# Kernel optimization log

Hardware: AMD Instinct MI355X
Metric: run time of the kernel (lower is better)

Reference implementation:

```python
import jax, jax.numpy as jnp
import numpy as np

# nodes per graph before / after pool1 / after pool2 (111, ceil(.5*111)=56, ceil(.5*56)=28)
N0, N1, N2 = 111, 56, 28


def _gcn(x, adj, w):
    n = x.shape[1]
    a = adj + jnp.eye(n, dtype=x.dtype)
    d = a.sum(-1)
    dis = jnp.where(d > 0, jax.lax.rsqrt(d), 0.0)
    an = dis[:, :, None] * a * dis[:, None, :]
    return jnp.einsum('bij,bjf->bif', an, x @ w)


def _cheb(x, adj, wk):
    # ChebConv K=3 (the 'sp' spectral branch; K=3 is set in __init__), lmax=2
    # => scaled Laplacian L_hat = L - I = -D^-1/2 A D^-1/2
    d = adj.sum(-1)
    dis = jnp.where(d > 0, jax.lax.rsqrt(d), 0.0)
    lh = -(dis[:, :, None] * adj * dis[:, None, :])
    t1 = jnp.einsum('bij,bjf->bif', lh, x)
    t2 = 2.0 * jnp.einsum('bij,bjf->bif', lh, t1) - x
    return x @ wk[0] + t1 @ wk[1] + t2 @ wk[2]


def _pool(x, adj, k):
    # HGPSLPool (sl=False): node information score = ||(I - D^-1 A) x||_1 per node,
    # top-k node selection per graph, induced subgraph on the kept nodes.
    d = adj.sum(-1)
    dinv = jnp.where(d > 0, 1.0 / d, 0.0)
    h = x - dinv[..., None] * jnp.einsum('bij,bjf->bif', adj, x)
    score = jnp.abs(h).sum(-1)                      # [B, N]
    _, idx = jax.lax.top_k(score, k)                # [B, k]
    xp = jnp.take_along_axis(x, idx[..., None], axis=1)
    rows = jnp.take_along_axis(adj, idx[..., None], axis=1)
    adjp = jnp.take_along_axis(rows, idx[:, None, :], axis=2)
    return xp, adjp


def _readout(h):
    # cat[global_max_pool, global_mean_pool] over the node axis
    return jnp.concatenate([h.max(axis=1), h.mean(axis=1)], axis=-1)


def _forward(x, adj, w_gcn1, w_sp1, w_gcn2, w_sp2, lin1_w, lin1_b, lin2_w, lin2_b):
    xm = jax.nn.relu(_gcn(x, adj, w_gcn1))
    xp = jax.nn.relu(_cheb(x, adj, w_sp1))
    h = jnp.concatenate([xm, xp], axis=-1)          # [B, 111, 256]
    h, adj1 = _pool(h, adj, N1)                     # [B, 56, 256]
    x1 = _readout(h)                                # [B, 512]
    xm = jax.nn.relu(_gcn(h, adj1, w_gcn2))
    xp = jax.nn.relu(_cheb(h, adj1, w_sp2))
    h = jnp.concatenate([xm, xp], axis=-1)          # [B, 56, 256]
    h, adj2 = _pool(h, adj1, N2)                    # [B, 28, 256]
    x2 = _readout(h)                                # [B, 512]
    flat = h.reshape(h.shape[0], -1)                # [B, 28*256]
    z = jnp.concatenate([flat, x1, x2], axis=-1)    # [B, 8192]
    f = jax.nn.relu(z @ lin1_w + lin1_b)
    features = jax.nn.relu(f @ lin2_w + lin2_b)
    x_lo = jax.nn.softmax(features, axis=-1)
    return x_lo, features


def setup_inputs() -> dict:
    B, F, D2, NHID = 2048, 111, 128, 256
    key = jax.random.key(0)
    ks = jax.random.split(key, 8)
    x = jax.random.normal(ks[0], (B, N0, F), jnp.float32)
    u = jax.random.uniform(ks[1], (B, N0, N0), jnp.float32)
    a = (u < 0.15).astype(jnp.float32)
    adj = jnp.maximum(a, jnp.transpose(a, (0, 2, 1))) * (1.0 - jnp.eye(N0, dtype=jnp.float32))
    s = 0.05
    w_gcn1 = jax.random.normal(ks[2], (F, D2), jnp.float32) * s
    w_sp1 = jax.random.normal(ks[3], (3, F, D2), jnp.float32) * s
    w_gcn2 = jax.random.normal(ks[4], (2 * D2, D2), jnp.float32) * s
    w_sp2 = jax.random.normal(ks[5], (3, 2 * D2, D2), jnp.float32) * s
    din = (N2 + 4) * 2 * D2  # 8192: flattened pooled nodes + two max/mean readouts
    lin1_w = jax.random.normal(ks[6], (din, NHID), jnp.float32) * s
    lin1_b = jnp.zeros((NHID,), jnp.float32)
    lin2_w = jax.random.normal(ks[7], (NHID, NHID // 2), jnp.float32) * s
    lin2_b = jnp.zeros((NHID // 2,), jnp.float32)
    return {'x': x, 'adj': adj, 'w_gcn1': w_gcn1, 'w_sp1': w_sp1, 'w_gcn2': w_gcn2,
            'w_sp2': w_sp2, 'lin1_w': lin1_w, 'lin1_b': lin1_b, 'lin2_w': lin2_w, 'lin2_b': lin2_b}


def reference(x, adj, w_gcn1, w_sp1, w_gcn2, w_sp2, lin1_w, lin1_b, lin2_w, lin2_b):
    return _forward(x, adj, w_gcn1, w_sp1, w_gcn2, w_sp2, lin1_w, lin1_b, lin2_w, lin2_b)
```

## Files before the change

kernel.cpp:

```cpp
#include <hip/hip_runtime.h>
#include <hip/hip_bf16.h>

#define NB   2048
#define NN0  111
#define NN1  56
#define NN2  28
#define FD   256
#define HD   128

__global__ __launch_bounds__(512, 2) void k_stage1(
    const float* __restrict__ x, const float* __restrict__ adj,
    const float* __restrict__ wg, const float* __restrict__ wsp,
    float* __restrict__ h1, int* __restrict__ selb,
    unsigned long long* __restrict__ adjp, int b0)
{
  extern __shared__ float sm[];
  float* xs   = sm;
  float* bufw = xs + 12432;
  unsigned* abits = (unsigned*)(bufw + 14336);
  float* dis0 = (float*)(abits + 448);
  float* dis1 = dis0 + 112;
  float* dinv = dis1 + 112;
  float* sc   = dinv + 112;
  int*   sel  = (int*)(sc + 112);

  const int tid  = threadIdx.x;
  const int lane = tid & 63;
  const int wv   = tid >> 6;
  const int bl   = blockIdx.x;
  const int b    = b0 + bl;
  const float* xb = x   + (size_t)b * (NN0 * NN0);
  const float* ab = adj + (size_t)b * (NN0 * NN0);

  for (int idx = tid; idx < NN0 * NN0; idx += 512) {
    int i = idx / NN0, k = idx - i * NN0;
    xs[i * 112 + k] = xb[idx];
  }
  if (tid < 128) bufw[111 * 128 + tid] = 0.0f;
  for (int i = wv; i < NN0; i += 8) {
    unsigned long long m0 = __ballot(ab[i * NN0 + lane] != 0.0f);
    float a1v = (64 + lane < NN0) ? ab[i * NN0 + 64 + lane] : 0.0f;
    unsigned long long m1 = __ballot(a1v != 0.0f);
    if (lane == 0) {
      abits[i * 4 + 0] = (unsigned)m0; abits[i * 4 + 1] = (unsigned)(m0 >> 32);
      abits[i * 4 + 2] = (unsigned)m1; abits[i * 4 + 3] = (unsigned)(m1 >> 32);
      int d = __popcll(m0) + __popcll(m1);
      dis0[i] = (d > 0) ? (1.0f / sqrtf((float)d)) : 0.0f;
      dis1[i] = 1.0f / sqrtf((float)(d + 1));
      dinv[i] = (d > 0) ? (1.0f / (float)d) : 0.0f;
    }
  }
  __syncthreads();

  auto nsum2 = [&](int i) {
    const unsigned* rb = abits + i * 4;
    unsigned lo0 = (unsigned)__builtin_amdgcn_readfirstlane(rb[0]);
    unsigned hi0 = (unsigned)__builtin_amdgcn_readfirstlane(rb[1]);
    unsigned lo1 = (unsigned)__builtin_amdgcn_readfirstlane(rb[2]);
    unsigned hi1 = (unsigned)__builtin_amdgcn_readfirstlane(rb[3]);
    unsigned long long u0 = ((unsigned long long)hi0 << 32) | (unsigned long long)lo0;
    unsigned long long u1 = ((unsigned long long)hi1 << 32) | (unsigned long long)lo1;
    float2 s0 = {0,0}, s1 = {0,0}, s2 = {0,0}, s3 = {0,0};
    while (u0 | u1) {
      int j0 = u0 ? (int)__builtin_ctzll(u0) : 111; u0 &= u0 - 1;
      int j1 = u0 ? (int)__builtin_ctzll(u0) : 111; u0 &= u0 - 1;
      int j2 = u1 ? (int)(64 + __builtin_ctzll(u1)) : 111; u1 &= u1 - 1;
      int j3 = u1 ? (int)(64 + __builtin_ctzll(u1)) : 111; u1 &= u1 - 1;
      float2 p0 = *(const float2*)&bufw[j0 * 128 + 2 * lane];
      float2 p1 = *(const float2*)&bufw[j1 * 128 + 2 * lane];
      float2 p2 = *(const float2*)&bufw[j2 * 128 + 2 * lane];
      float2 p3 = *(const float2*)&bufw[j3 * 128 + 2 * lane];
      s0.x += p0.x; s0.y += p0.y; s1.x += p1.x; s1.y += p1.y;
      s2.x += p2.x; s2.y += p2.y; s3.x += p3.x; s3.y += p3.y;
    }
    return make_float2((s0.x + s1.x) + (s2.x + s3.x),
                       (s0.y + s1.y) + (s2.y + s3.y));
  };

  float* h1b = h1 + (size_t)bl * (NN0 * FD);

  {
    float aG0[14], aG1[14];
    float a2r[2][14], a1r[2][14], a0r[2][14];
#pragma unroll
    for (int t = 0; t < 14; ++t) {
      aG0[t] = 0.f; aG1[t] = 0.f;
      a2r[0][t] = 0.f; a2r[1][t] = 0.f;
      a1r[0][t] = 0.f; a1r[1][t] = 0.f;
      a0r[0][t] = 0.f; a0r[1][t] = 0.f;
    }
    const float* pG = wg  + 2 * lane;
    const float* p2 = wsp + 2 * (NN0 * HD) + 2 * lane;
    const float* p1 = wsp + 1 * (NN0 * HD) + 2 * lane;
    const float* p0 = wsp + 2 * lane;
    for (int kq = 0; kq < 27; ++kq) {
      int k0 = kq * 4;
      float2 g[4], s2[4], u1w[4], v0[4];
#pragma unroll
      for (int j = 0; j < 4; ++j) {
        g[j]   = *(const float2*)&pG[(k0 + j) * HD];
        s2[j]  = *(const float2*)&p2[(k0 + j) * HD];
        u1w[j] = *(const float2*)&p1[(k0 + j) * HD];
        v0[j]  = *(const float2*)&p0[(k0 + j) * HD];
      }
#pragma unroll
      for (int t = 0; t < 14; ++t) {
        int r = wv + 8 * t;
        if (r < NN0) {
          float4 xq = *(const float4*)(xs + r * 112 + k0);
          aG0[t]    += xq.x*g[0].x   + xq.y*g[1].x   + xq.z*g[2].x   + xq.w*g[3].x;
          aG1[t]    += xq.x*g[0].y   + xq.y*g[1].y   + xq.z*g[2].y   + xq.w*g[3].y;
          a2r[0][t] += xq.x*s2[0].x  + xq.y*s2[1].x  + xq.z*s2[2].x  + xq.w*s2[3].x;
          a2r[1][t] += xq.x*s2[0].y  + xq.y*s2[1].y  + xq.z*s2[2].y  + xq.w*s2[3].y;
          a1r[0][t] += xq.x*u1w[0].x + xq.y*u1w[1].x + xq.z*u1w[2].x + xq.w*u1w[3].x;
          a1r[1][t] += xq.x*u1w[0].y + xq.y*u1w[1].y + xq.z*u1w[2].y + xq.w*u1w[3].y;
          a0r[0][t] += xq.x*v0[0].x  + xq.y*v0[1].x  + xq.z*v0[2].x  + xq.w*v0[3].x;
          a0r[1][t] += xq.x*v0[0].y  + xq.y*v0[1].y  + xq.z*v0[2].y  + xq.w*v0[3].y;
        }
      }
    }
#pragma unroll
    for (int k = 108; k < 111; ++k) {
      float2 gv = *(const float2*)&pG[k * HD];
      float2 sv = *(const float2*)&p2[k * HD];
      float2 uv = *(const float2*)&p1[k * HD];
      float2 vv = *(const float2*)&p0[k * HD];
#pragma unroll
      for (int t = 0; t < 14; ++t) {
        int r = wv + 8 * t;
        if (r < NN0) {
          float xv = xs[r * 112 + k];
          aG0[t]    += xv * gv.x; aG1[t]    += xv * gv.y;
          a2r[0][t] += xv * sv.x; a2r[1][t] += xv * sv.y;
          a1r[0][t] += xv * uv.x; a1r[1][t] += xv * uv.y;
          a0r[0][t] += xv * vv.x; a0r[1][t] += xv * vv.y;
        }
      }
    }
#pragma unroll
    for (int t = 0; t < 14; ++t) {
      int r = wv + 8 * t;
      if (r < NN0) {
        float d1 = dis1[r];
        *(float2*)&bufw[r * 128 + 2 * lane] = make_float2(d1 * aG0[t], d1 * aG1[t]);
      }
    }
    __syncthreads();

    for (int t = 0; t < 14; ++t) {
      int i = wv + 8 * t;
      if (i < NN0) {
        float2 self = *(const float2*)&bufw[i * 128 + 2 * lane];
        float2 ns = nsum2(i);
        float d1 = dis1[i];
        float2 o = make_float2(fmaxf(d1 * (self.x + ns.x), 0.f),
                               fmaxf(d1 * (self.y + ns.y), 0.f));
        *(float2*)&h1b[i * FD + 2 * lane] = o;
      }
    }
    __syncthreads();
#pragma unroll
    for (int t = 0; t < 14; ++t) {
      int r = wv + 8 * t;
      if (r < NN0) {
        float d0r = dis0[r];
        *(float2*)&bufw[r * 128 + 2 * lane] = make_float2(d0r * a2r[0][t], d0r * a2r[1][t]);
      }
    }
    __syncthreads();
    float2 ur[14], cacc[14];
    for (int t = 0; t < 14; ++t) {
      int i = wv + 8 * t;
      if (i < NN0) {
        float2 ns = nsum2(i);
        float sc0 = -dis0[i] * dis0[i];
        ur[t] = make_float2(sc0 * ns.x, sc0 * ns.y);
        cacc[t] = make_float2(-a2r[0][t], -a2r[1][t]);
      } else { ur[t] = make_float2(0.f, 0.f); cacc[t] = make_float2(0.f, 0.f); }
    }
    __syncthreads();
#pragma unroll
    for (int t = 0; t < 14; ++t) {
      int r = wv + 8 * t;
      if (r < NN0) *(float2*)&bufw[r * 128 + 2 * lane] = ur[t];
    }
    __syncthreads();
    for (int t = 0; t < 14; ++t) {
      int i = wv + 8 * t;
      if (i < NN0) {
        float2 ns = nsum2(i);
        float d0i = dis0[i];
        cacc[t].x -= 2.0f * d0i * ns.x;
        cacc[t].y -= 2.0f * d0i * ns.y;
      }
    }
    __syncthreads();
#pragma unroll
    for (int t = 0; t < 14; ++t) {
      int r = wv + 8 * t;
      if (r < NN0) {
        float d0r = dis0[r];
        *(float2*)&bufw[r * 128 + 2 * lane] = make_float2(d0r * a1r[0][t], d0r * a1r[1][t]);
      }
    }
    __syncthreads();
    for (int t = 0; t < 14; ++t) {
      int i = wv + 8 * t;
      if (i < NN0) {
        float2 ns = nsum2(i);
        float d0i = dis0[i];
        float2 o = make_float2(fmaxf(cacc[t].x - d0i * ns.x + a0r[0][t], 0.f),
                               fmaxf(cacc[t].y - d0i * ns.y + a0r[1][t], 0.f));
        *(float2*)&h1b[i * FD + HD + 2 * lane] = o;
      }
    }
  }
  __syncthreads();

  float sA[14];
#pragma unroll
  for (int t = 0; t < 14; ++t) {
    int r = wv + 8 * t;
    if (r < NN0)
      *(float2*)&bufw[r * 128 + 2 * lane] = *(const float2*)&h1b[r * FD + 2 * lane];
  }
  __syncthreads();
  for (int t = 0; t < 14; ++t) {
    int i = wv + 8 * t;
    if (i < NN0) {
      float2 self = *(const float2*)&bufw[i * 128 + 2 * lane];
      float2 nb = nsum2(i);
      float di = dinv[i];
      sA[t] = fabsf(self.x - di * nb.x) + fabsf(self.y - di * nb.y);
    } else sA[t] = 0.f;
  }
  __syncthreads();
#pragma unroll
  for (int t = 0; t < 14; ++t) {
    int r = wv + 8 * t;
    if (r < NN0)
      *(float2*)&bufw[r * 128 + 2 * lane] = *(const float2*)&h1b[r * FD + HD + 2 * lane];
  }
  __syncthreads();
  for (int t = 0; t < 14; ++t) {
    int i = wv + 8 * t;
    if (i < NN0) {
      float2 self = *(const float2*)&bufw[i * 128 + 2 * lane];
      float2 nb = nsum2(i);
      float di = dinv[i];
      float s = sA[t] + fabsf(self.x - di * nb.x) + fabsf(self.y - di * nb.y);
      for (int off = 32; off; off >>= 1) s += __shfl_xor(s, off);
      if (lane == 0) sc[i] = s;
    }
  }
  __syncthreads();
  if (tid < NN0) {
    float my = sc[tid];
    int cnt = 0;
    for (int j = 0; j < NN0; ++j) {
      float sj = sc[j];
      cnt += (sj > my) || (sj == my && j < tid);
    }
    if (cnt < NN1) sel[cnt] = tid;
  }
  __syncthreads();
  for (int r = wv; r < NN1; r += 8) {
    int i = sel[r];
    int j2 = (lane < NN1) ? sel[lane] : 0;
    bool bit = (lane < NN1) && ((abits[i * 4 + (j2 >> 5)] >> (j2 & 31)) & 1);
    unsigned long long m = __ballot(bit);
    if (lane == 0) adjp[(size_t)bl * NN1 + r] = m;
  }
  if (tid < NN1) selb[(size_t)bl * NN1 + tid] = sel[tid];
}

__global__ __launch_bounds__(512, 2) void k_stage2(
    const float* __restrict__ h1, const int* __restrict__ selb,
    const unsigned long long* __restrict__ adjp,
    const float* __restrict__ wg, const float* __restrict__ wsp,
    float* __restrict__ zbuf)
{
  extern __shared__ float sm[];
  float* hs   = sm;
  float* bufw = hs + 14592;
  unsigned long long* rowm = (unsigned long long*)(bufw + 7296);
  float* dis0 = (float*)(rowm + 56);
  float* dis1 = dis0 + 64;
  float* dinv = dis1 + 64;
  float* sc   = dinv + 64;
  int* sel2   = (int*)(sc + 64);
  int* seli   = sel2 + 32;

  const int tid = threadIdx.x, lane = tid & 63, wv = tid >> 6;
  const int bl = blockIdx.x;
  const float* h1b = h1 + (size_t)bl * (NN0 * FD);
  float* zb = zbuf + (size_t)bl * 8192;

  if (tid < NN1) seli[tid] = selb[(size_t)bl * NN1 + tid];
  if (tid < 128) bufw[56 * 128 + tid] = 0.0f;
  if (tid < 256) hs[56 * 256 + tid] = 0.0f;
  if (tid < NN1) {
    unsigned long long m = adjp[(size_t)bl * NN1 + tid];
    rowm[tid] = m;
    int d = __popcll(m);
    dis0[tid] = (d > 0) ? (1.0f / sqrtf((float)d)) : 0.0f;
    dis1[tid] = 1.0f / sqrtf((float)(d + 1));
    dinv[tid] = (d > 0) ? (1.0f / (float)d) : 0.0f;
  }
  __syncthreads();
  for (int q = tid; q < NN1 * 64; q += 512) {
    int row = q >> 6, c = q & 63;
    ((float4*)hs)[row * 64 + c] =
        ((const float4*)(h1b + (size_t)seli[row] * FD))[c];
  }
  __syncthreads();
  if (tid < FD) {
    float mx = -3.402823466e38f, sm2 = 0.0f;
    for (int r = 0; r < NN1; ++r) {
      float v = hs[r * 256 + tid];
      mx = fmaxf(mx, v); sm2 += v;
    }
    zb[7168 + tid] = mx;
    zb[7424 + tid] = sm2 / 56.0f;
  }

  auto nsum2 = [&](int i) {
    unsigned long long m = rowm[i];
    unsigned lo = (unsigned)__builtin_amdgcn_readfirstlane((unsigned)m);
    unsigned hi = (unsigned)__builtin_amdgcn_readfirstlane((unsigned)(m >> 32));
    unsigned long long u = ((unsigned long long)hi << 32) | (unsigned long long)lo;
    float2 s0 = {0,0}, s1 = {0,0}, s2 = {0,0}, s3 = {0,0};
    while (u) {
      int j0 = (int)__builtin_ctzll(u); u &= u - 1;
      int j1 = u ? (int)__builtin_ctzll(u) : 56; u &= u - 1;
      int j2 = u ? (int)__builtin_ctzll(u) : 56; u &= u - 1;
      int j3 = u ? (int)__builtin_ctzll(u) : 56; u &= u - 1;
      float2 p0 = *(const float2*)&bufw[j0 * 128 + 2 * lane];
      float2 p1 = *(const float2*)&bufw[j1 * 128 + 2 * lane];
      float2 p2 = *(const float2*)&bufw[j2 * 128 + 2 * lane];
      float2 p3 = *(const float2*)&bufw[j3 * 128 + 2 * lane];
      s0.x += p0.x; s0.y += p0.y; s1.x += p1.x; s1.y += p1.y;
      s2.x += p2.x; s2.y += p2.y; s3.x += p3.x; s3.y += p3.y;
    }
    return make_float2((s0.x + s1.x) + (s2.x + s3.x),
                       (s0.y + s1.y) + (s2.y + s3.y));
  };
  auto nsum_hs = [&](int i, int base) {
    unsigned long long m = rowm[i];
    unsigned lo = (unsigned)__builtin_amdgcn_readfirstlane((unsigned)m);
    unsigned hi = (unsigned)__builtin_amdgcn_readfirstlane((unsigned)(m >> 32));
    unsigned long long u = ((unsigned long long)hi << 32) | (unsigned long long)lo;
    float2 s0 = {0,0}, s1 = {0,0}, s2 = {0,0}, s3 = {0,0};
    while (u) {
      int j0 = (int)__builtin_ctzll(u); u &= u - 1;
      int j1 = u ? (int)__builtin_ctzll(u) : 56; u &= u - 1;
      int j2 = u ? (int)__builtin_ctzll(u) : 56; u &= u - 1;
      int j3 = u ? (int)__builtin_ctzll(u) : 56; u &= u - 1;
      float2 p0 = *(const float2*)&hs[j0 * 256 + base + 2 * lane];
      float2 p1 = *(const float2*)&hs[j1 * 256 + base + 2 * lane];
      float2 p2 = *(const float2*)&hs[j2 * 256 + base + 2 * lane];
      float2 p3 = *(const float2*)&hs[j3 * 256 + base + 2 * lane];
      s0.x += p0.x; s0.y += p0.y; s1.x += p1.x; s1.y += p1.y;
      s2.x += p2.x; s2.y += p2.y; s3.x += p3.x; s3.y += p3.y;
    }
    return make_float2((s0.x + s1.x) + (s2.x + s3.x),
                       (s0.y + s1.y) + (s2.y + s3.y));
  };

  float aG0[7], aG1[7];
  float a2r[2][7], a1r[2][7], a0r[2][7];
#pragma unroll
  for (int t = 0; t < 7; ++t) {
    aG0[t] = 0.f; aG1[t] = 0.f;
    a2r[0][t] = 0.f; a2r[1][t] = 0.f;
    a1r[0][t] = 0.f; a1r[1][t] = 0.f;
    a0r[0][t] = 0.f; a0r[1][t] = 0.f;
  }
  {
    const float* pG = wg  + 2 * lane;
    const float* p2 = wsp + 2 * (FD * HD) + 2 * lane;
    const float* p1 = wsp + 1 * (FD * HD) + 2 * lane;
    const float* p0 = wsp + 2 * lane;
    for (int kq = 0; kq < 64; ++kq) {
      int k0 = kq * 4;
      float2 g[4], s2[4], u1w[4], v0[4];
#pragma unroll
      for (int j = 0; j < 4; ++j) {
        g[j]   = *(const float2*)&pG[(k0 + j) * HD];
        s2[j]  = *(const float2*)&p2[(k0 + j) * HD];
        u1w[j] = *(const float2*)&p1[(k0 + j) * HD];
        v0[j]  = *(const float2*)&p0[(k0 + j) * HD];
      }
#pragma unroll
      for (int t = 0; t < 7; ++t) {
        int r = wv + 8 * t;
        float4 xq = *(const float4*)(hs + r * 256 + k0);
        aG0[t]    += xq.x*g[0].x   + xq.y*g[1].x   + xq.z*g[2].x   + xq.w*g[3].x;
        aG1[t]    += xq.x*g[0].y   + xq.y*g[1].y   + xq.z*g[2].y   + xq.w*g[3].y;
        a2r[0][t] += xq.x*s2[0].x  + xq.y*s2[1].x  + xq.z*s2[2].x  + xq.w*s2[3].x;
        a2r[1][t] += xq.x*s2[0].y  + xq.y*s2[1].y  + xq.z*s2[2].y  + xq.w*s2[3].y;
        a1r[0][t] += xq.x*u1w[0].x + xq.y*u1w[1].x + xq.z*u1w[2].x + xq.w*u1w[3].x;
        a1r[1][t] += xq.x*u1w[0].y + xq.y*u1w[1].y + xq.z*u1w[2].y + xq.w*u1w[3].y;
        a0r[0][t] += xq.x*v0[0].x  + xq.y*v0[1].x  + xq.z*v0[2].x  + xq.w*v0[3].x;
        a0r[1][t] += xq.x*v0[0].y  + xq.y*v0[1].y  + xq.z*v0[2].y  + xq.w*v0[3].y;
      }
    }
#pragma unroll
    for (int t = 0; t < 7; ++t) {
      int r = wv + 8 * t;
      float d1 = dis1[r];
      *(float2*)&bufw[r * 128 + 2 * lane] = make_float2(d1 * aG0[t], d1 * aG1[t]);
    }
  }
  __syncthreads();
  float2 ho[7];
#pragma unroll
  for (int t = 0; t < 7; ++t) {
    int i = wv + 8 * t;
    float2 self = *(const float2*)&bufw[i * 128 + 2 * lane];
    float2 ns = nsum2(i);
    float d1 = dis1[i];
    float2 o = make_float2(fmaxf(d1 * (self.x + ns.x), 0.f),
                           fmaxf(d1 * (self.y + ns.y), 0.f));
    *(float2*)&hs[i * 256 + 2 * lane] = o;
    ho[t] = o;
  }
  __syncthreads();
  float sA[7];
#pragma unroll
  for (int t = 0; t < 7; ++t) {
    int i = wv + 8 * t;
    float2 nb = nsum_hs(i, 0);
    float di = dinv[i];
    sA[t] = fabsf(ho[t].x - di * nb.x) + fabsf(ho[t].y - di * nb.y);
  }
#pragma unroll
  for (int t = 0; t < 7; ++t) {
    int r = wv + 8 * t;
    float d0r = dis0[r];
    *(float2*)&bufw[r * 128 + 2 * lane] = make_float2(d0r * a2r[0][t], d0r * a2r[1][t]);
  }
  __syncthreads();
  float2 ur[7], cacc[7];
#pragma unroll
  for (int t = 0; t < 7; ++t) {
    int i = wv + 8 * t;
    float2 ns = nsum2(i);
    float sc0 = -dis0[i] * dis0[i];
    ur[t] = make_float2(sc0 * ns.x, sc0 * ns.y);
    cacc[t] = make_float2(-a2r[0][t], -a2r[1][t]);
  }
  __syncthreads();
#pragma unroll
  for (int t = 0; t < 7; ++t) {
    int r = wv + 8 * t;
    *(float2*)&bufw[r * 128 + 2 * lane] = ur[t];
  }
  __syncthreads();
#pragma unroll
  for (int t = 0; t < 7; ++t) {
    int i = wv + 8 * t;
    float2 ns = nsum2(i);
    float d0i = dis0[i];
    cacc[t].x -= 2.0f * d0i * ns.x;
    cacc[t].y -= 2.0f * d0i * ns.y;
  }
  __syncthreads();
#pragma unroll
  for (int t = 0; t < 7; ++t) {
    int r = wv + 8 * t;
    float d0r = dis0[r];
    *(float2*)&bufw[r * 128 + 2 * lane] = make_float2(d0r * a1r[0][t], d0r * a1r[1][t]);
  }
  __syncthreads();
#pragma unroll
  for (int t = 0; t < 7; ++t) {
    int i = wv + 8 * t;
    float2 ns = nsum2(i);
    float d0i = dis0[i];
    float2 o = make_float2(fmaxf(cacc[t].x - d0i * ns.x + a0r[0][t], 0.f),
                           fmaxf(cacc[t].y - d0i * ns.y + a0r[1][t], 0.f));
    *(float2*)&hs[i * 256 + 128 + 2 * lane] = o;
    cacc[t] = o;
  }
  __syncthreads();
#pragma unroll
  for (int t = 0; t < 7; ++t) {
    int i = wv + 8 * t;
    float2 nb = nsum_hs(i, 128);
    float di = dinv[i];
    float s = sA[t] + fabsf(cacc[t].x - di * nb.x) + fabsf(cacc[t].y - di * nb.y);
    for (int off = 32; off; off >>= 1) s += __shfl_xor(s, off);
    if (lane == 0) sc[i] = s;
  }
  __syncthreads();
  if (tid < NN1) {
    float my = sc[tid];
    int cnt = 0;
    for (int j = 0; j < NN1; ++j) {
      float sj = sc[j];
      cnt += (sj > my) || (sj == my && j < tid);
    }
    if (cnt < NN2) sel2[cnt] = tid;
  }
  __syncthreads();
  for (int r = wv; r < NN2; r += 8) {
    const float* hr = hs + sel2[r] * 256 + lane;
    float* dst = zb + r * 256 + lane;
    dst[0] = hr[0]; dst[64] = hr[64]; dst[128] = hr[128]; dst[192] = hr[192];
  }
  if (tid < FD) {
    float mx = -3.402823466e38f, sm2 = 0.0f;
    for (int r = 0; r < NN2; ++r) {
      float v = hs[sel2[r] * 256 + tid];
      mx = fmaxf(mx, v); sm2 += v;
    }
    zb[7680 + tid] = mx;
    zb[7936 + tid] = sm2 / 28.0f;
  }
}

__global__ __launch_bounds__(512) void k_lin1f(
    const float* __restrict__ zbuf, const float* __restrict__ w,
    const float* __restrict__ bias, float* __restrict__ fbuf)
{
  __shared__ float smem[8576];
  float* wt = smem;
  float* zt = smem + 8320;

  const int tid = threadIdx.x;
  const int col = tid & 63;
  const int ksub = tid >> 6;
  const int g0 = blockIdx.x * 8;
  const int gz = tid >> 5, kz = tid & 31;

  float acc[8][4];
#pragma unroll
  for (int g = 0; g < 8; ++g)
#pragma unroll
    for (int c = 0; c < 4; ++c) acc[g][c] = 0.f;

  const float* wbase = w + (size_t)ksub * 256 + col * 4;
  const float* zbase = zbuf + (size_t)(g0 + gz) * 8192 + kz;

  float4 wr4[4]; float zr1 = 0.f;
#pragma unroll
  for (int q = 0; q < 4; ++q)
    wr4[q] = *(const float4*)(wbase + (size_t)(8 * q) * 256);
  if (tid < 256) zr1 = zbase[0];
#pragma unroll
  for (int q = 0; q < 4; ++q)
    *(float4*)&wt[(ksub + 8 * q) * 260 + col * 4] = wr4[q];
  if (tid < 256) zt[kz * 8 + gz] = zr1;
  __syncthreads();

  for (int it = 0; it < 256; ++it) {
    if (it + 1 < 256) {
      const float* wn = wbase + (size_t)(it + 1) * 32 * 256;
#pragma unroll
      for (int q = 0; q < 4; ++q)
        wr4[q] = *(const float4*)(wn + (size_t)(8 * q) * 256);
      if (tid < 256) zr1 = zbase[(it + 1) * 32];
    }
#pragma unroll
    for (int kk = 0; kk < 4; ++kk) {
      int k = ksub * 4 + kk;
      float4 za = *(const float4*)&zt[k * 8];
      float4 zb = *(const float4*)&zt[k * 8 + 4];
      float4 wv = *(const float4*)&wt[k * 260 + col * 4];
      acc[0][0] += za.x * wv.x; acc[0][1] += za.x * wv.y; acc[0][2] += za.x * wv.z; acc[0][3] += za.x * wv.w;
      acc[1][0] += za.y * wv.x; acc[1][1] += za.y * wv.y; acc[1][2] += za.y * wv.z; acc[1][3] += za.y * wv.w;
      acc[2][0] += za.z * wv.x; acc[2][1] += za.z * wv.y; acc[2][2] += za.z * wv.z; acc[2][3] += za.z * wv.w;
      acc[3][0] += za.w * wv.x; acc[3][1] += za.w * wv.y; acc[3][2] += za.w * wv.z; acc[3][3] += za.w * wv.w;
      acc[4][0] += zb.x * wv.x; acc[4][1] += zb.x * wv.y; acc[4][2] += zb.x * wv.z; acc[4][3] += zb.x * wv.w;
      acc[5][0] += zb.y * wv.x; acc[5][1] += zb.y * wv.y; acc[5][2] += zb.y * wv.z; acc[5][3] += zb.y * wv.w;
      acc[6][0] += zb.z * wv.x; acc[6][1] += zb.z * wv.y; acc[6][2] += zb.z * wv.z; acc[6][3] += zb.z * wv.w;
      acc[7][0] += zb.w * wv.x; acc[7][1] += zb.w * wv.y; acc[7][2] += zb.w * wv.z; acc[7][3] += zb.w * wv.w;
    }
    __syncthreads();
    if (it + 1 < 256) {
#pragma unroll
      for (int q = 0; q < 4; ++q)
        *(float4*)&wt[(ksub + 8 * q) * 260 + col * 4] = wr4[q];
      if (tid < 256) zt[kz * 8 + gz] = zr1;
      __syncthreads();
    }
  }

  float* red = smem;
  for (int half = 4; half >= 1; half >>= 1) {
    if (ksub >= half && ksub < 2 * half) {
      float* dst = red + ((ksub - half) * 64 + col) * 33;
#pragma unroll
      for (int g = 0; g < 8; ++g)
#pragma unroll
        for (int c = 0; c < 4; ++c) dst[g * 4 + c] = acc[g][c];
    }
    __syncthreads();
    if (ksub < half) {
      const float* src = red + (ksub * 64 + col) * 33;
#pragma unroll
      for (int g = 0; g < 8; ++g)
#pragma unroll
        for (int c = 0; c < 4; ++c) acc[g][c] += src[g * 4 + c];
    }
    __syncthreads();
  }
  if (ksub == 0) {
    float4 bv = *(const float4*)(bias + col * 4);
#pragma unroll
    for (int g = 0; g < 8; ++g) {
      float4 o;
      o.x = fmaxf(acc[g][0] + bv.x, 0.f);
      o.y = fmaxf(acc[g][1] + bv.y, 0.f);
      o.z = fmaxf(acc[g][2] + bv.z, 0.f);
      o.w = fmaxf(acc[g][3] + bv.w, 0.f);
      *(float4*)&fbuf[(size_t)(g0 + g) * 256 + col * 4] = o;
    }
  }
}

__global__ __launch_bounds__(128) void k_head(
    const float* __restrict__ fbuf, const float* __restrict__ w2,
    const float* __restrict__ b2, float* __restrict__ out, int b0)
{
  __shared__ __align__(16) float fs[256];
  __shared__ float red[2];
  const int tid = threadIdx.x, lane = tid & 63, wv = tid >> 6;
  const int bl = blockIdx.x, b = b0 + bl;
  for (int i = tid; i < 256; i += 128) fs[i] = fbuf[(size_t)bl * 256 + i];
  __syncthreads();
  float acc = b2[tid];
  for (int k = 0; k < 256; k += 4) {
    float4 fq = *(const float4*)(fs + k);
    acc += fq.x * w2[(k + 0) * 128 + tid] + fq.y * w2[(k + 1) * 128 + tid]
         + fq.z * w2[(k + 2) * 128 + tid] + fq.w * w2[(k + 3) * 128 + tid];
  }
  float feat = fmaxf(acc, 0.0f);
  out[(size_t)(NB * 128) + (size_t)b * 128 + tid] = feat;
  float m = feat;
  for (int off = 32; off; off >>= 1) m = fmaxf(m, __shfl_xor(m, off));
  if (lane == 0) red[wv] = m;
  __syncthreads();
  m = fmaxf(red[0], red[1]);
  float e = expf(feat - m);
  float s = e;
  for (int off = 32; off; off >>= 1) s += __shfl_xor(s, off);
  __syncthreads();
  if (lane == 0) red[wv] = s;
  __syncthreads();
  s = red[0] + red[1];
  out[(size_t)b * 128 + tid] = e / s;
}

extern "C" void kernel_launch(void* const* d_in, const int* in_sizes, int n_in,
                              void* d_out, int out_size, void* d_ws, size_t ws_size,
                              hipStream_t stream) {
  const float* x    = (const float*)d_in[0];
  const float* adj  = (const float*)d_in[1];
  const float* wg1  = (const float*)d_in[2];
  const float* wsp1 = (const float*)d_in[3];
  const float* wg2  = (const float*)d_in[4];
  const float* wsp2 = (const float*)d_in[5];
  const float* l1w  = (const float*)d_in[6];
  const float* l1b  = (const float*)d_in[7];
  const float* l2w  = (const float*)d_in[8];
  const float* l2b  = (const float*)d_in[9];
  float* out = (float*)d_out;

  auto al = [](size_t v) { return (v + 255) & ~(size_t)255; };
  size_t oh1, oselb, oadjp, oz, of;
  auto plan = [&](int g) -> size_t {
    size_t o = 0;
    oh1 = o;   o += al((size_t)g * NN0 * FD * 4);
    oselb = o; o += al((size_t)g * NN1 * 4);
    oadjp = o; o += al((size_t)g * NN1 * 8);
    oz = o;    o += al((size_t)g * 8192 * 4);
    of = o;    o += al((size_t)g * FD * 4);
    return o;
  };
  int G = 2048;
  while (G > 64 && plan(G) > ws_size) G >>= 1;
  if (plan(G) > ws_size) return;

  char* wsb = (char*)d_ws;
  float* h1  = (float*)(wsb + oh1);
  int* selb  = (int*)(wsb + oselb);
  unsigned long long* adjp = (unsigned long long*)(wsb + oadjp);
  float* zbuf = (float*)(wsb + oz);
  float* fbuf = (float*)(wsb + of);

  const size_t LDS1 = (size_t)(12432 + 14336 + 448 + 112 + 112 + 112 + 112 + 64) * 4;
  const size_t LDS2 = (size_t)(14592 + 7296 + 112 + 64 + 64 + 64 + 64 + 32 + 64) * 4;

  for (int b0 = 0; b0 < NB; b0 += G) {
    k_stage1<<<G, 512, LDS1, stream>>>(x, adj, wg1, wsp1, h1, selb, adjp, b0);
    k_stage2<<<G, 512, LDS2, stream>>>(h1, selb, adjp, wg2, wsp2, zbuf);
    k_lin1f<<<G / 8, 512, 0, stream>>>(zbuf, l1w, l1b, fbuf);
    k_head<<<G, 128, 0, stream>>>(fbuf, l2w, l2b, out, b0);
  }
}
```

Measured before the change: 3.269 ms.

## Split stage-1 kernel: move pooling score and top-k selection into separate kernel

Splits the first stage so the GCN/Cheb convolution kernel ends after writing h1, and a new k_sel kernel handles the pooling score, top-k selection and induced adjacency. The adjacency bitmask is written to global workspace so k_sel can rebuild degrees and neighbour sums. The aim is to shrink per-kernel register and LDS pressure so each kernel can sustain higher occupancy. The cost is an extra launch, re-reading h1 from global memory and extra workspace traffic for the bitmasks.

```diff
diff --git a/kernel.cpp b/kernel.cpp
--- a/kernel.cpp
+++ b/kernel.cpp
@@ -11,8 +11,7 @@
 __global__ __launch_bounds__(512, 2) void k_stage1(
     const float* __restrict__ x, const float* __restrict__ adj,
     const float* __restrict__ wg, const float* __restrict__ wsp,
-    float* __restrict__ h1, int* __restrict__ selb,
-    unsigned long long* __restrict__ adjp, int b0)
+    float* __restrict__ h1, unsigned* __restrict__ abg, int b0)
 {
   extern __shared__ float sm[];
   float* xs   = sm;
@@ -20,9 +19,6 @@
   unsigned* abits = (unsigned*)(bufw + 14336);
   float* dis0 = (float*)(abits + 448);
   float* dis1 = dis0 + 112;
-  float* dinv = dis1 + 112;
-  float* sc   = dinv + 112;
-  int*   sel  = (int*)(sc + 112);
 
   const int tid  = threadIdx.x;
   const int lane = tid & 63;
@@ -37,6 +33,7 @@
     xs[i * 112 + k] = xb[idx];
   }
   if (tid < 128) bufw[111 * 128 + tid] = 0.0f;
+  if (tid >= 444 && tid < 448) abits[tid] = 0u;
   for (int i = wv; i < NN0; i += 8) {
     unsigned long long m0 = __ballot(ab[i * NN0 + lane] != 0.0f);
     float a1v = (64 + lane < NN0) ? ab[i * NN0 + 64 + lane] : 0.0f;
@@ -47,10 +44,10 @@
       int d = __popcll(m0) + __popcll(m1);
       dis0[i] = (d > 0) ? (1.0f / sqrtf((float)d)) : 0.0f;
       dis1[i] = 1.0f / sqrtf((float)(d + 1));
-      dinv[i] = (d > 0) ? (1.0f / (float)d) : 0.0f;
-    }
-  }
-  __syncthreads();
+    }
+  }
+  __syncthreads();
+  for (int q = tid; q < 448; q += 512) abg[(size_t)bl * 448 + q] = abits[q];
 
   auto nsum2 = [&](int i) {
     const unsigned* rb = abits + i * 4;
@@ -79,16 +76,16 @@
 
   float* h1b = h1 + (size_t)bl * (NN0 * FD);
 
+  float aG0[14], aG1[14];
+  float a2r[2][14], a1r[2][14], a0r[2][14];
+#pragma unroll
+  for (int t = 0; t < 14; ++t) {
+    aG0[t] = 0.f; aG1[t] = 0.f;
+    a2r[0][t] = 0.f; a2r[1][t] = 0.f;
+    a1r[0][t] = 0.f; a1r[1][t] = 0.f;
+    a0r[0][t] = 0.f; a0r[1][t] = 0.f;
+  }
   {
-    float aG0[14], aG1[14];
-    float a2r[2][14], a1r[2][14], a0r[2][14];
-#pragma unroll
-    for (int t = 0; t < 14; ++t) {
-      aG0[t] = 0.f; aG1[t] = 0.f;
-      a2r[0][t] = 0.f; a2r[1][t] = 0.f;
-      a1r[0][t] = 0.f; a1r[1][t] = 0.f;
-      a0r[0][t] = 0.f; a0r[1][t] = 0.f;
-    }
     const float* pG = wg  + 2 * lane;
     const float* p2 = wsp + 2 * (NN0 * HD) + 2 * lane;
     const float* p1 = wsp + 1 * (NN0 * HD) + 2 * lane;
@@ -145,79 +142,127 @@
         *(float2*)&bufw[r * 128 + 2 * lane] = make_float2(d1 * aG0[t], d1 * aG1[t]);
       }
     }
-    __syncthreads();
-
-    for (int t = 0; t < 14; ++t) {
-      int i = wv + 8 * t;
-      if (i < NN0) {
-        float2 self = *(const float2*)&bufw[i * 128 + 2 * lane];
-        float2 ns = nsum2(i);
-        float d1 = dis1[i];
-        float2 o = make_float2(fmaxf(d1 * (self.x + ns.x), 0.f),
-                               fmaxf(d1 * (self.y + ns.y), 0.f));
-        *(float2*)&h1b[i * FD + 2 * lane] = o;
-      }
-    }
-    __syncthreads();
-#pragma unroll
-    for (int t = 0; t < 14; ++t) {
-      int r = wv + 8 * t;
-      if (r < NN0) {
-        float d0r = dis0[r];
-        *(float2*)&bufw[r * 128 + 2 * lane] = make_float2(d0r * a2r[0][t], d0r * a2r[1][t]);
-      }
-    }
-    __syncthreads();
-    float2 ur[14], cacc[14];
-    for (int t = 0; t < 14; ++t) {
-      int i = wv + 8 * t;
-      if (i < NN0) {
-        float2 ns = nsum2(i);
-        float sc0 = -dis0[i] * dis0[i];
-        ur[t] = make_float2(sc0 * ns.x, sc0 * ns.y);
-        cacc[t] = make_float2(-a2r[0][t], -a2r[1][t]);
-      } else { ur[t] = make_float2(0.f, 0.f); cacc[t] = make_float2(0.f, 0.f); }
-    }
-    __syncthreads();
-#pragma unroll
-    for (int t = 0; t < 14; ++t) {
-      int r = wv + 8 * t;
-      if (r < NN0) *(float2*)&bufw[r * 128 + 2 * lane] = ur[t];
-    }
-    __syncthreads();
-    for (int t = 0; t < 14; ++t) {
-      int i = wv + 8 * t;
-      if (i < NN0) {
-        float2 ns = nsum2(i);
-        float d0i = dis0[i];
-        cacc[t].x -= 2.0f * d0i * ns.x;
-        cacc[t].y -= 2.0f * d0i * ns.y;
-      }
-    }
-    __syncthreads();
-#pragma unroll
-    for (int t = 0; t < 14; ++t) {
-      int r = wv + 8 * t;
-      if (r < NN0) {
-        float d0r = dis0[r];
-        *(float2*)&bufw[r * 128 + 2 * lane] = make_float2(d0r * a1r[0][t], d0r * a1r[1][t]);
-      }
-    }
-    __syncthreads();
-    for (int t = 0; t < 14; ++t) {
-      int i = wv + 8 * t;
-      if (i < NN0) {
-        float2 ns = nsum2(i);
-        float d0i = dis0[i];
-        float2 o = make_float2(fmaxf(cacc[t].x - d0i * ns.x + a0r[0][t], 0.f),
-                               fmaxf(cacc[t].y - d0i * ns.y + a0r[1][t], 0.f));
-        *(float2*)&h1b[i * FD + HD + 2 * lane] = o;
-      }
-    }
-  }
-  __syncthreads();
-
-  float sA[14];
+  }
+  __syncthreads();
+
+  for (int t = 0; t < 14; ++t) {
+    int i = wv + 8 * t;
+    if (i < NN0) {
+      float2 self = *(const float2*)&bufw[i * 128 + 2 * lane];
+      float2 ns = nsum2(i);
+      float d1 = dis1[i];
+      float2 o = make_float2(fmaxf(d1 * (self.x + ns.x), 0.f),
+                             fmaxf(d1 * (self.y + ns.y), 0.f));
+      *(float2*)&h1b[i * FD + 2 * lane] = o;
+    }
+  }
+  __syncthreads();
+#pragma unroll
+  for (int t = 0; t < 14; ++t) {
+    int r = wv + 8 * t;
+    if (r < NN0) {
+      float d0r = dis0[r];
+      *(float2*)&bufw[r * 128 + 2 * lane] = make_float2(d0r * a2r[0][t], d0r * a2r[1][t]);
+    }
+  }
+  __syncthreads();
+  float2 ur[14], cacc[14];
+  for (int t = 0; t < 14; ++t) {
+    int i = wv + 8 * t;
+    if (i < NN0) {
+      float2 ns = nsum2(i);
+      float sc0 = -dis0[i] * dis0[i];
+      ur[t] = make_float2(sc0 * ns.x, sc0 * ns.y);
+      cacc[t] = make_float2(-a2r[0][t], -a2r[1][t]);
+    } else { ur[t] = make_float2(0.f, 0.f); cacc[t] = make_float2(0.f, 0.f); }
+  }
+  __syncthreads();
+#pragma unroll
+  for (int t = 0; t < 14; ++t) {
+    int r = wv + 8 * t;
+    if (r < NN0) *(float2*)&bufw[r * 128 + 2 * lane] = ur[t];
+  }
+  __syncthreads();
+  for (int t = 0; t < 14; ++t) {
+    int i = wv + 8 * t;
+    if (i < NN0) {
+      float2 ns = nsum2(i);
+      float d0i = dis0[i];
+      cacc[t].x -= 2.0f * d0i * ns.x;
+      cacc[t].y -= 2.0f * d0i * ns.y;
+    }
+  }
+  __syncthreads();
+#pragma unroll
+  for (int t = 0; t < 14; ++t) {
+    int r = wv + 8 * t;
+    if (r < NN0) {
+      float d0r = dis0[r];
+      *(float2*)&bufw[r * 128 + 2 * lane] = make_float2(d0r * a1r[0][t], d0r * a1r[1][t]);
+    }
+  }
+  __syncthreads();
+  for (int t = 0; t < 14; ++t) {
+    int i = wv + 8 * t;
+    if (i < NN0) {
+      float2 ns = nsum2(i);
+      float d0i = dis0[i];
+      float2 o = make_float2(fmaxf(cacc[t].x - d0i * ns.x + a0r[0][t], 0.f),
+                             fmaxf(cacc[t].y - d0i * ns.y + a0r[1][t], 0.f));
+      *(float2*)&h1b[i * FD + HD + 2 * lane] = o;
+    }
+  }
+}
+
+__global__ __launch_bounds__(512) void k_sel(
+    const float* __restrict__ h1, const unsigned* __restrict__ abg,
+    int* __restrict__ selb, unsigned long long* __restrict__ adjp, int)
+{
+  extern __shared__ float sm[];
+  float* bufw = sm;
+  unsigned* abits = (unsigned*)(bufw + 14336);
+  float* dinv = (float*)(abits + 448);
+  float* sc   = dinv + 112;
+  int*   sel  = (int*)(sc + 112);
+
+  const int tid = threadIdx.x, lane = tid & 63, wv = tid >> 6;
+  const int bl = blockIdx.x;
+  const float* h1b = h1 + (size_t)bl * (NN0 * FD);
+
+  for (int q = tid; q < 448; q += 512) abits[q] = abg[(size_t)bl * 448 + q];
+  if (tid < 128) bufw[111 * 128 + tid] = 0.0f;
+  __syncthreads();
+  if (tid < NN0) {
+    int d = __popc(abits[tid*4]) + __popc(abits[tid*4+1])
+          + __popc(abits[tid*4+2]) + __popc(abits[tid*4+3]);
+    dinv[tid] = (d > 0) ? (1.0f / (float)d) : 0.0f;
+  }
+
+  auto nsum2 = [&](int i) {
+    const unsigned* rb = abits + i * 4;
+    unsigned lo0 = (unsigned)__builtin_amdgcn_readfirstlane(rb[0]);
+    unsigned hi0 = (unsigned)__builtin_amdgcn_readfirstlane(rb[1]);
+    unsigned lo1 = (unsigned)__builtin_amdgcn_readfirstlane(rb[2]);
+    unsigned hi1 = (unsigned)__builtin_amdgcn_readfirstlane(rb[3]);
+    unsigned long long u0 = ((unsigned long long)hi0 << 32) | (unsigned long long)lo0;
+    unsigned long long u1 = ((unsigned long long)hi1 << 32) | (unsigned long long)lo1;
+    float2 s0 = {0,0}, s1 = {0,0}, s2 = {0,0}, s3 = {0,0};
+    while (u0 | u1) {
+      int j0 = u0 ? (int)__builtin_ctzll(u0) : 111; u0 &= u0 - 1;
+      int j1 = u0 ? (int)__builtin_ctzll(u0) : 111; u0 &= u0 - 1;
+      int j2 = u1 ? (int)(64 + __builtin_ctzll(u1)) : 111; u1 &= u1 - 1;
+      int j3 = u1 ? (int)(64 + __builtin_ctzll(u1)) : 111; u1 &= u1 - 1;
+      float2 p0 = *(const float2*)&bufw[j0 * 128 + 2 * lane];
+      float2 p1 = *(const float2*)&bufw[j1 * 128 + 2 * lane];
+      float2 p2 = *(const float2*)&bufw[j2 * 128 + 2 * lane];
+      float2 p3 = *(const float2*)&bufw[j3 * 128 + 2 * lane];
+      s0.x += p0.x; s0.y += p0.y; s1.x += p1.x; s1.y += p1.y;
+      s2.x += p2.x; s2.y += p2.y; s3.x += p3.x; s3.y += p3.y;
+    }
+    return make_float2((s0.x + s1.x) + (s2.x + s3.x),
+                       (s0.y + s1.y) + (s2.y + s3.y));
+  };
+
 #pragma unroll
   for (int t = 0; t < 14; ++t) {
     int r = wv + 8 * t;
@@ -225,6 +270,7 @@
       *(float2*)&bufw[r * 128 + 2 * lane] = *(const float2*)&h1b[r * FD + 2 * lane];
   }
   __syncthreads();
+  float sA[14];
   for (int t = 0; t < 14; ++t) {
     int i = wv + 8 * t;
     if (i < NN0) {
@@ -669,10 +715,11 @@
   float* out = (float*)d_out;
 
   auto al = [](size_t v) { return (v + 255) & ~(size_t)255; };
-  size_t oh1, oselb, oadjp, oz, of;
+  size_t oh1, oabg, oselb, oadjp, oz, of;
   auto plan = [&](int g) -> size_t {
     size_t o = 0;
     oh1 = o;   o += al((size_t)g * NN0 * FD * 4);
+    oabg = o;  o += al((size_t)g * 448 * 4);
     oselb = o; o += al((size_t)g * NN1 * 4);
     oadjp = o; o += al((size_t)g * NN1 * 8);
     oz = o;    o += al((size_t)g * 8192 * 4);
@@ -685,16 +732,19 @@
 
   char* wsb = (char*)d_ws;
   float* h1  = (float*)(wsb + oh1);
+  unsigned* abg = (unsigned*)(wsb + oabg);
   int* selb  = (int*)(wsb + oselb);
   unsigned long long* adjp = (unsigned long long*)(wsb + oadjp);
   float* zbuf = (float*)(wsb + oz);
   float* fbuf = (float*)(wsb + of);
 
-  const size_t LDS1 = (size_t)(12432 + 14336 + 448 + 112 + 112 + 112 + 112 + 64) * 4;
+  const size_t LDS1 = (size_t)(12432 + 14336 + 448 + 112 + 112) * 4;
+  const size_t LDSS = (size_t)(14336 + 448 + 112 + 112 + 64) * 4;
   const size_t LDS2 = (size_t)(14592 + 7296 + 112 + 64 + 64 + 64 + 64 + 32 + 64) * 4;
 
   for (int b0 = 0; b0 < NB; b0 += G) {
-    k_stage1<<<G, 512, LDS1, stream>>>(x, adj, wg1, wsp1, h1, selb, adjp, b0);
+    k_stage1<<<G, 512, LDS1, stream>>>(x, adj, wg1, wsp1, h1, abg, b0);
+    k_sel<<<G, 512, LDSS, stream>>>(h1, abg, selb, adjp, b0);
     k_stage2<<<G, 512, LDS2, stream>>>(h1, selb, adjp, wg2, wsp2, zbuf);
     k_lin1f<<<G / 8, 512, 0, stream>>>(zbuf, l1w, l1b, fbuf);
     k_head<<<G, 128, 0, stream>>>(fbuf, l2w, l2b, out, b0);
```

Result: faster. 3.159 ms (-3.4%).
